# Optimization experiments

Measured on AMD Instinct MI355X. Metric: run time of the kernel, lower is better.

The kernel has to match this reference:

```python
import jax, jax.numpy as jnp
import numpy as np

ALPHA = 0.2  # leaky_relu negative slope
NEG = -1e12


def setup_inputs() -> dict:
    key = jax.random.key(0)
    k1, k2, k3, k4 = jax.random.split(key, 4)
    N, FIN, FOUT = 8192, 128, 64
    inp = jax.random.normal(k1, (N, FIN), dtype=jnp.float32)
    adj = jax.random.randint(k2, (N, N), 0, 2, dtype=jnp.int32)
    W = jax.random.normal(k3, (FIN, FOUT), dtype=jnp.float32) * 0.1
    a = jax.random.normal(k4, (2 * FOUT, 1), dtype=jnp.float32) * 0.1
    return {"inp": inp, "adj": adj, "W": W, "a": a}


def reference(inp, adj, W, a):
    # h: [N, F]
    h = inp @ W
    F = h.shape[1]
    # additive decomposition of a^T [h_i ; h_j] = (h @ a1)_i + (h @ a2)_j
    a1 = a[:F, 0]
    a2 = a[F:, 0]
    s1 = h @ a1  # [N]
    s2 = h @ a2  # [N]
    e = jax.nn.leaky_relu(s1[:, None] + s2[None, :], negative_slope=ALPHA)  # [N, N]
    att = jnp.where(adj > 0, e, jnp.float32(NEG))
    att = jax.nn.softmax(att, axis=1)
    # dropout is identity in eval mode (training=False)
    h_prime = att @ h  # [N, F]
    return jax.nn.elu(h_prime)  # concat=True
```

## Files before the change

kernel.cpp:

```cpp
#include <hip/hip_runtime.h>

typedef __attribute__((ext_vector_type(8))) short short8;
typedef __attribute__((ext_vector_type(4))) float f32x4;
typedef __attribute__((ext_vector_type(4))) int   i32x4;
typedef unsigned long long u64;

#define NN 8192
#define FIN 128
#define FOUT 64
#define LRELU_ALPHA 0.2f

__device__ __forceinline__ unsigned short f2bf(float x) {
    unsigned u = __float_as_uint(x);
    unsigned r = (u + 0x7FFFu + ((u >> 16) & 1u)) >> 16;
    return (unsigned short)r;
}

__device__ __forceinline__ unsigned vcol_of(unsigned i) {
    return (i & ~63u) | ((i & 3u) << 4) | ((i & 63u) >> 2);
}

__global__ __launch_bounds__(256) void gat_prep(
    const float* __restrict__ inp, const float* __restrict__ W,
    const float* __restrict__ a,
    unsigned short* __restrict__ htp, float* __restrict__ s1, float* __restrict__ s2,
    float* __restrict__ e1v, float* __restrict__ e2v)
{
    __shared__ float Wl[FIN * FOUT];
    __shared__ float il[4 * FIN];
    const int tid = threadIdx.x;
    const int i0 = blockIdx.x * 4;

    #pragma unroll
    for (int k = 0; k < (FIN * FOUT) / 256; ++k)
        Wl[tid + 256 * k] = W[tid + 256 * k];
    #pragma unroll
    for (int k = 0; k < (4 * FIN) / 256; ++k)
        il[tid + 256 * k] = inp[(size_t)i0 * FIN + tid + 256 * k];
    __syncthreads();

    const int r = tid >> 6;
    const int f = tid & 63;
    float acc = 0.f;
    #pragma unroll 8
    for (int k = 0; k < FIN; ++k)
        acc = fmaf(il[r * FIN + k], Wl[k * FOUT + f], acc);

    float v1 = acc * a[f];
    float v2 = acc * a[FOUT + f];
    #pragma unroll
    for (int off = 32; off; off >>= 1) {
        v1 += __shfl_xor(v1, off, 64);
        v2 += __shfl_xor(v2, off, 64);
    }
    const int i = i0 + r;
    const unsigned vc = vcol_of((unsigned)i);
    if (f == 0) {
        s1[i] = v1;
        s2[i] = v2;
        e1v[vc] = __expf(v2);
        e2v[vc] = __expf(LRELU_ALPHA * v2);
    }
    const unsigned Tt = vc >> 6, ic = vc & 63u;
    const unsigned ss = ic >> 5, kk = (ic >> 3) & 3u, ee = ic & 7u;
    const unsigned fb = (unsigned)f >> 4, ll = (unsigned)f & 15u;
    htp[((Tt * 8u + ss * 4u + fb) << 9) + ((kk * 16u + ll) << 3) + ee] = f2bf(acc);
}

__global__ __launch_bounds__(1024) void gat_s2max(const float* __restrict__ s2,
                                                  float* __restrict__ s2m)
{
    __shared__ float red[16];
    float m = -1e30f;
    for (int idx = threadIdx.x; idx < NN; idx += 1024) m = fmaxf(m, s2[idx]);
    #pragma unroll
    for (int off = 32; off; off >>= 1) m = fmaxf(m, __shfl_xor(m, off, 64));
    if ((threadIdx.x & 63) == 0) red[threadIdx.x >> 6] = m;
    __syncthreads();
    if (threadIdx.x == 0) {
        float mm = red[0];
        #pragma unroll
        for (int k = 1; k < 16; ++k) mm = fmaxf(mm, red[k]);
        s2m[0] = mm;
    }
}

#define ADJ_ISSUE(P, tt) do {                                                 \
    const unsigned oa_ = vadj0 + (unsigned)(tt) * 256u;                       \
    asm volatile("global_load_dwordx4 %0, %1, %2"                             \
                 : "=v"(P##0) : "v"(oa_), "s"(adjb));                         \
    asm volatile("global_load_dwordx4 %0, %1, %2"                             \
                 : "=v"(P##1) : "v"(oa_ + 131072u), "s"(adjb));               \
    asm volatile("global_load_dwordx4 %0, %1, %2"                             \
                 : "=v"(P##2) : "v"(oa_ + 262144u), "s"(adjb));               \
    asm volatile("global_load_dwordx4 %0, %1, %2"                             \
                 : "=v"(P##3) : "v"(oa_ + 393216u), "s"(adjb));               \
} while (0)

#define HTP_ISSUE(P, tt) do {                                                 \
    const unsigned oh_  = vhtp0 + (unsigned)(tt) * 8192u;                     \
    const unsigned oh2_ = oh_ + 4096u;                                        \
    asm volatile("global_load_dwordx4 %0, %1, %2 offset:0"                    \
                 : "=v"(P##_h0) : "v"(oh_), "s"(htpb));                       \
    asm volatile("global_load_dwordx4 %0, %1, %2 offset:1024"                 \
                 : "=v"(P##_h1) : "v"(oh_), "s"(htpb));                       \
    asm volatile("global_load_dwordx4 %0, %1, %2 offset:2048"                 \
                 : "=v"(P##_h2) : "v"(oh_), "s"(htpb));                       \
    asm volatile("global_load_dwordx4 %0, %1, %2 offset:3072"                 \
                 : "=v"(P##_h3) : "v"(oh_), "s"(htpb));                       \
    asm volatile("global_load_dwordx4 %0, %1, %2 offset:0"                    \
                 : "=v"(P##_h4) : "v"(oh2_), "s"(htpb));                      \
    asm volatile("global_load_dwordx4 %0, %1, %2 offset:1024"                 \
                 : "=v"(P##_h5) : "v"(oh2_), "s"(htpb));                      \
    asm volatile("global_load_dwordx4 %0, %1, %2 offset:2048"                 \
                 : "=v"(P##_h6) : "v"(oh2_), "s"(htpb));                      \
    asm volatile("global_load_dwordx4 %0, %1, %2 offset:3072"                 \
                 : "=v"(P##_h7) : "v"(oh2_), "s"(htpb));                      \
} while (0)

#define BALLOT1(V, rr, MBL, MBH) do {                                         \
    const u64 b0_ = __ballot(V[0] > 0);                                       \
    const u64 b1_ = __ballot(V[1] > 0);                                       \
    const u64 b2_ = __ballot(V[2] > 0);                                       \
    const u64 b3_ = __ballot(V[3] > 0);                                       \
    const u64 sA_ = (kg & 2) ? b1_ : b0_;                                     \
    const u64 sB_ = (kg & 2) ? b3_ : b2_;                                     \
    const unsigned m0_ = (unsigned)(sA_ >> sh) & 0xffu;                       \
    const unsigned m1_ = (unsigned)(sB_ >> sh) & 0xffu;                       \
    MBL = (myr == (rr)) ? m0_ : MBL;                                          \
    MBH = (myr == (rr)) ? m1_ : MBH;                                          \
} while (0)

#define BALLOT4(P, MBL, MBH) do {                                             \
    BALLOT1(P##0, 0, MBL, MBH);                                               \
    BALLOT1(P##1, 1, MBL, MBH);                                               \
    BALLOT1(P##2, 2, MBL, MBH);                                               \
    BALLOT1(P##3, 3, MBL, MBH);                                               \
} while (0)

#define COMPUTE(B0_, B1_, B2_, B3_, MB, uu) do {                              \
    const int eo_ = (uu) * 32 + 8 * kg;                                       \
    const f32x4 E1a_ = *(const f32x4*)&e1l[eo_];                              \
    const f32x4 E1b_ = *(const f32x4*)&e1l[eo_ + 4];                          \
    const f32x4 E2a_ = *(const f32x4*)&e2l[eo_];                              \
    const f32x4 E2b_ = *(const f32x4*)&e2l[eo_ + 4];                          \
    float p_[8];                                                              \
    _Pragma("unroll")                                                         \
    for (int e = 0; e < 8; ++e) {                                             \
        const float e1_ = (e < 4) ? E1a_[e] : E1b_[e - 4];                    \
        const float e2_ = (e < 4) ? E2a_[e] : E2b_[e - 4];                    \
        const float pv_ = fmaxf(c1 * e1_, c2 * e2_);                          \
        p_[e] = (((MB) >> e) & 1u) ? pv_ : 0.f;                               \
        lsum += p_[e];                                                        \
    }                                                                         \
    union { short8 s8; unsigned u4[4]; } afu_;                                \
    _Pragma("unroll")                                                         \
    for (int q = 0; q < 4; ++q) {                                             \
        unsigned rr_;                                                         \
        asm("v_cvt_pk_bf16_f32 %0, %1, %2"                                    \
            : "=v"(rr_) : "v"(p_[2 * q]), "v"(p_[2 * q + 1]));                \
        afu_.u4[q] = rr_;                                                     \
    }                                                                         \
    acc0 = __builtin_amdgcn_mfma_f32_16x16x32_bf16(afu_.s8, B0_, acc0, 0,0,0);\
    acc1 = __builtin_amdgcn_mfma_f32_16x16x32_bf16(afu_.s8, B1_, acc1, 0,0,0);\
    acc2 = __builtin_amdgcn_mfma_f32_16x16x32_bf16(afu_.s8, B2_, acc2, 0,0,0);\
    acc3 = __builtin_amdgcn_mfma_f32_16x16x32_bf16(afu_.s8, B3_, acc3, 0,0,0);\
} while (0)

#define ITER(P, tt, W) do {                                                   \
    asm volatile("s_waitcnt vmcnt(" #W ")" ::: "memory");                     \
    __builtin_amdgcn_sched_barrier(0);                                        \
    unsigned mbl_ = 0, mbh_ = 0;                                              \
    BALLOT4(P, mbl_, mbh_);                                                   \
    if ((tt) + 2 < nt) ADJ_ISSUE(P, (tt) + 2);                                \
    COMPUTE(P##_h0, P##_h1, P##_h2, P##_h3, mbl_, 2 * (tt));                  \
    COMPUTE(P##_h4, P##_h5, P##_h6, P##_h7, mbh_, 2 * (tt) + 1);              \
    if ((tt) + 2 < nt) HTP_ISSUE(P, (tt) + 2);                                \
} while (0)

__global__ __launch_bounds__(256, 2) void gat_attn(
    const int* __restrict__ adj, const unsigned short* __restrict__ htp,
    const float* __restrict__ s1, const float* __restrict__ e1v,
    const float* __restrict__ e2v, const float* __restrict__ s2m,
    float* __restrict__ pacc, float* __restrict__ pl, int jlen)
{
    __shared__ float e1l[2048];
    __shared__ float e2l[2048];

    const int w    = threadIdx.x >> 6;
    const int lane = threadIdx.x & 63;
    const int lo   = lane & 15;
    const int kg   = lane >> 4;
    const int i0   = blockIdx.x * 64;
    const int i    = i0 + w * 16 + lo;
    const int jstart = blockIdx.y * jlen;
    const int nt     = jlen >> 6;

    for (int x = threadIdx.x; x < (jlen >> 2); x += 256) {
        ((f32x4*)e1l)[x] = *(const f32x4*)(e1v + jstart + 4 * x);
        ((f32x4*)e2l)[x] = *(const f32x4*)(e2v + jstart + 4 * x);
    }
    __syncthreads();

    const float s1v = s1[i];
    const float mm  = s1v + s2m[0];
    const float Mi  = fmaxf(mm, LRELU_ALPHA * mm);
    const float c1  = __expf(s1v - Mi);
    const float c2  = __expf(LRELU_ALPHA * s1v - Mi);

    const int      myr = lo >> 2;
    const unsigned sh  = ((lo & 3) << 4) | ((kg & 1) << 3);

    const int* adjb = adj + (size_t)i0 * NN;
    const unsigned short* htpb = htp;
    const unsigned vadj0 = (unsigned)((((w * 16 + kg) * NN) + (lane & 15) * 4 + jstart) * 4);
    const unsigned vhtp0 = (unsigned)(((unsigned)(jstart >> 6) * 8192u) + lane * 16);

    f32x4 acc0 = {0.f,0.f,0.f,0.f}, acc1 = {0.f,0.f,0.f,0.f};
    f32x4 acc2 = {0.f,0.f,0.f,0.f}, acc3 = {0.f,0.f,0.f,0.f};
    float lsum = 0.f;

    i32x4 X0, X1, X2, X3, Y0, Y1, Y2, Y3;
    short8 X_h0, X_h1, X_h2, X_h3, X_h4, X_h5, X_h6, X_h7;
    short8 Y_h0, Y_h1, Y_h2, Y_h3, Y_h4, Y_h5, Y_h6, Y_h7;

    __builtin_amdgcn_sched_barrier(0);
    ADJ_ISSUE(X, 0); HTP_ISSUE(X, 0);
    ADJ_ISSUE(Y, 1); HTP_ISSUE(Y, 1);

    for (int k2 = 0; k2 < nt / 2 - 1; ++k2) {
        const int t0 = 2 * k2;
        ITER(X, t0, 12);
        ITER(Y, t0 + 1, 12);
    }
    ITER(X, nt - 2, 12);
    ITER(Y, nt - 1, 0);

    lsum += __shfl_xor(lsum, 16, 64);
    lsum += __shfl_xor(lsum, 32, 64);
    if (kg == 0)
        pl[(size_t)blockIdx.y * NN + i] = lsum;

    float* pa = pacc + ((size_t)blockIdx.y * NN + i0 + w * 16) * FOUT;
    #pragma unroll
    for (int reg = 0; reg < 4; ++reg) {
        const int orow = kg * 4 + reg;
        pa[(size_t)orow * FOUT + 0 * 16 + lo] = acc0[reg];
        pa[(size_t)orow * FOUT + 1 * 16 + lo] = acc1[reg];
        pa[(size_t)orow * FOUT + 2 * 16 + lo] = acc2[reg];
        pa[(size_t)orow * FOUT + 3 * 16 + lo] = acc3[reg];
    }
}

__global__ __launch_bounds__(256) void gat_reduce(
    const float* __restrict__ pacc, const float* __restrict__ pl,
    float* __restrict__ out, int JS)
{
    const int q = blockIdx.x * 256 + threadIdx.x;
    const int i = q >> 4;
    float l = 0.f;
    f32x4 v = {0.f, 0.f, 0.f, 0.f};
    for (int js = 0; js < JS; ++js) {
        l += pl[(size_t)js * NN + i];
        const f32x4 pv = *(const f32x4*)(pacc + (size_t)js * NN * FOUT + 4 * q);
        v[0] += pv[0]; v[1] += pv[1]; v[2] += pv[2]; v[3] += pv[3];
    }
    const float rl = 1.f / l;
    f32x4 o;
    #pragma unroll
    for (int e = 0; e < 4; ++e) {
        const float r = v[e] * rl;
        o[e] = r > 0.f ? r : expm1f(r);
    }
    *(f32x4*)(out + 4 * q) = o;
}

extern "C" void kernel_launch(void* const* d_in, const int* in_sizes, int n_in,
                              void* d_out, int out_size, void* d_ws, size_t ws_size,
                              hipStream_t stream)
{
    const float* inp = (const float*)d_in[0];
    const int*   adj = (const int*)d_in[1];
    const float* W   = (const float*)d_in[2];
    const float* a   = (const float*)d_in[3];
    float* out = (float*)d_out;

    char* ws = (char*)d_ws;
    unsigned short* htp = (unsigned short*)ws; ws += (size_t)FOUT * NN * 2;
    float* s1  = (float*)ws; ws += (size_t)NN * 4;
    float* s2  = (float*)ws; ws += (size_t)NN * 4;
    float* e1v = (float*)ws; ws += (size_t)NN * 4;
    float* e2v = (float*)ws; ws += (size_t)NN * 4;
    float* s2m = (float*)ws; ws += 256;
    const size_t fixed = (size_t)(ws - (char*)d_ws);

    int JS = 8;
    while (JS > 4 && fixed + (size_t)JS * NN * 4ull * (FOUT + 1) > ws_size) JS >>= 1;
    const int jlen = NN / JS;

    float* pl   = (float*)ws; ws += (size_t)JS * NN * 4;
    float* pacc = (float*)ws;

    gat_prep  <<<NN / 4, 256, 0, stream>>>(inp, W, a, htp, s1, s2, e1v, e2v);
    gat_s2max <<<1, 1024, 0, stream>>>(s2, s2m);
    gat_attn  <<<dim3(NN / 64, JS), 256, 0, stream>>>(adj, htp, s1, e1v, e2v, s2m, pacc, pl, jlen);
    gat_reduce<<<(NN * FOUT) / 1024, 256, 0, stream>>>(pacc, pl, out, JS);
}
```

Baseline: 87.30 us.

## Stage h tiles through LDS with direct global-to-LDS loads shared across waves

The attention kernel no longer has every wave load the full bf16 h tile into its own registers. Each wave now issues two direct global-to-LDS loads into a four-slot shared buffer, and all four waves read their MFMA B operands from LDS. This cuts redundant global traffic and register pressure, which may allow two blocks per CU. The cost is a workgroup barrier every iteration and LDS read traffic. The workspace-size fallback is removed and JS is fixed at 8, which could overflow a workspace that is too small.

```diff
diff --git a/kernel.cpp b/kernel.cpp
--- a/kernel.cpp
+++ b/kernel.cpp
@@ -14,6 +14,12 @@
     unsigned u = __float_as_uint(x);
     unsigned r = (u + 0x7FFFu + ((u >> 16) & 1u)) >> 16;
     return (unsigned short)r;
+}
+
+__device__ __forceinline__ void gl_lds16(const void* g, void* l) {
+    __builtin_amdgcn_global_load_lds(
+        (const __attribute__((address_space(1))) void*)g,
+        (__attribute__((address_space(3))) void*)l, 16, 0, 0);
 }
 
 __device__ __forceinline__ unsigned vcol_of(unsigned i) {
@@ -97,25 +103,12 @@
                  : "=v"(P##3) : "v"(oa_ + 393216u), "s"(adjb));               \
 } while (0)
 
-#define HTP_ISSUE(P, tt) do {                                                 \
-    const unsigned oh_  = vhtp0 + (unsigned)(tt) * 8192u;                     \
-    const unsigned oh2_ = oh_ + 4096u;                                        \
-    asm volatile("global_load_dwordx4 %0, %1, %2 offset:0"                    \
-                 : "=v"(P##_h0) : "v"(oh_), "s"(htpb));                       \
-    asm volatile("global_load_dwordx4 %0, %1, %2 offset:1024"                 \
-                 : "=v"(P##_h1) : "v"(oh_), "s"(htpb));                       \
-    asm volatile("global_load_dwordx4 %0, %1, %2 offset:2048"                 \
-                 : "=v"(P##_h2) : "v"(oh_), "s"(htpb));                       \
-    asm volatile("global_load_dwordx4 %0, %1, %2 offset:3072"                 \
-                 : "=v"(P##_h3) : "v"(oh_), "s"(htpb));                       \
-    asm volatile("global_load_dwordx4 %0, %1, %2 offset:0"                    \
-                 : "=v"(P##_h4) : "v"(oh2_), "s"(htpb));                      \
-    asm volatile("global_load_dwordx4 %0, %1, %2 offset:1024"                 \
-                 : "=v"(P##_h5) : "v"(oh2_), "s"(htpb));                      \
-    asm volatile("global_load_dwordx4 %0, %1, %2 offset:2048"                 \
-                 : "=v"(P##_h6) : "v"(oh2_), "s"(htpb));                      \
-    asm volatile("global_load_dwordx4 %0, %1, %2 offset:3072"                 \
-                 : "=v"(P##_h7) : "v"(oh2_), "s"(htpb));                      \
+#define ISSUE(P, tt) do {                                                     \
+    ADJ_ISSUE(P, tt);                                                         \
+    const unsigned short* g0_ = htpt + (size_t)(tt) * 4096 + (w * 2) * 512    \
+                                + lane * 8;                                   \
+    gl_lds16(g0_,       &hbuf[(tt) & 3][(w * 2) * 512]);                      \
+    gl_lds16(g0_ + 512, &hbuf[(tt) & 3][(w * 2 + 1) * 512]);                  \
 } while (0)
 
 #define BALLOT1(V, rr, MBL, MBH) do {                                         \
@@ -138,12 +131,16 @@
     BALLOT1(P##3, 3, MBL, MBH);                                               \
 } while (0)
 
-#define COMPUTE(B0_, B1_, B2_, B3_, MB, uu) do {                              \
+#define COMPUTE(HB, SB, MB, uu) do {                                          \
     const int eo_ = (uu) * 32 + 8 * kg;                                       \
     const f32x4 E1a_ = *(const f32x4*)&e1l[eo_];                              \
     const f32x4 E1b_ = *(const f32x4*)&e1l[eo_ + 4];                          \
     const f32x4 E2a_ = *(const f32x4*)&e2l[eo_];                              \
     const f32x4 E2b_ = *(const f32x4*)&e2l[eo_ + 4];                          \
+    const short8 B0_ = *(const short8*)((HB) + ((SB) * 4 + 0) * 512 + lane * 8); \
+    const short8 B1_ = *(const short8*)((HB) + ((SB) * 4 + 1) * 512 + lane * 8); \
+    const short8 B2_ = *(const short8*)((HB) + ((SB) * 4 + 2) * 512 + lane * 8); \
+    const short8 B3_ = *(const short8*)((HB) + ((SB) * 4 + 3) * 512 + lane * 8); \
     float p_[8];                                                              \
     _Pragma("unroll")                                                         \
     for (int e = 0; e < 8; ++e) {                                             \
@@ -170,12 +167,14 @@
 #define ITER(P, tt, W) do {                                                   \
     asm volatile("s_waitcnt vmcnt(" #W ")" ::: "memory");                     \
     __builtin_amdgcn_sched_barrier(0);                                        \
+    asm volatile("s_barrier" ::: "memory");                                   \
+    __builtin_amdgcn_sched_barrier(0);                                        \
     unsigned mbl_ = 0, mbh_ = 0;                                              \
     BALLOT4(P, mbl_, mbh_);                                                   \
-    if ((tt) + 2 < nt) ADJ_ISSUE(P, (tt) + 2);                                \
-    COMPUTE(P##_h0, P##_h1, P##_h2, P##_h3, mbl_, 2 * (tt));                  \
-    COMPUTE(P##_h4, P##_h5, P##_h6, P##_h7, mbh_, 2 * (tt) + 1);              \
-    if ((tt) + 2 < nt) HTP_ISSUE(P, (tt) + 2);                                \
+    const unsigned short* hb_ = &hbuf[(tt) & 3][0];                           \
+    COMPUTE(hb_, 0, mbl_, 2 * (tt));                                          \
+    COMPUTE(hb_, 1, mbh_, 2 * (tt) + 1);                                      \
+    if ((tt) + 2 < nt) ISSUE(P, (tt) + 2);                                    \
 } while (0)
 
 __global__ __launch_bounds__(256, 2) void gat_attn(
@@ -184,8 +183,9 @@
     const float* __restrict__ e2v, const float* __restrict__ s2m,
     float* __restrict__ pacc, float* __restrict__ pl, int jlen)
 {
-    __shared__ float e1l[2048];
-    __shared__ float e2l[2048];
+    __shared__ float e1l[1024];
+    __shared__ float e2l[1024];
+    __shared__ unsigned short hbuf[4][4096];
 
     const int w    = threadIdx.x >> 6;
     const int lane = threadIdx.x & 63;
@@ -212,28 +212,25 @@
     const unsigned sh  = ((lo & 3) << 4) | ((kg & 1) << 3);
 
     const int* adjb = adj + (size_t)i0 * NN;
-    const unsigned short* htpb = htp;
+    const unsigned short* htpt = htp + (size_t)(jstart >> 6) * 4096;
     const unsigned vadj0 = (unsigned)((((w * 16 + kg) * NN) + (lane & 15) * 4 + jstart) * 4);
-    const unsigned vhtp0 = (unsigned)(((unsigned)(jstart >> 6) * 8192u) + lane * 16);
 
     f32x4 acc0 = {0.f,0.f,0.f,0.f}, acc1 = {0.f,0.f,0.f,0.f};
     f32x4 acc2 = {0.f,0.f,0.f,0.f}, acc3 = {0.f,0.f,0.f,0.f};
     float lsum = 0.f;
 
     i32x4 X0, X1, X2, X3, Y0, Y1, Y2, Y3;
-    short8 X_h0, X_h1, X_h2, X_h3, X_h4, X_h5, X_h6, X_h7;
-    short8 Y_h0, Y_h1, Y_h2, Y_h3, Y_h4, Y_h5, Y_h6, Y_h7;
 
     __builtin_amdgcn_sched_barrier(0);
-    ADJ_ISSUE(X, 0); HTP_ISSUE(X, 0);
-    ADJ_ISSUE(Y, 1); HTP_ISSUE(Y, 1);
+    ISSUE(X, 0);
+    ISSUE(Y, 1);
 
     for (int k2 = 0; k2 < nt / 2 - 1; ++k2) {
         const int t0 = 2 * k2;
-        ITER(X, t0, 12);
-        ITER(Y, t0 + 1, 12);
-    }
-    ITER(X, nt - 2, 12);
+        ITER(X, t0, 6);
+        ITER(Y, t0 + 1, 6);
+    }
+    ITER(X, nt - 2, 6);
     ITER(Y, nt - 1, 0);
 
     lsum += __shfl_xor(lsum, 16, 64);
@@ -292,10 +289,8 @@
     float* e1v = (float*)ws; ws += (size_t)NN * 4;
     float* e2v = (float*)ws; ws += (size_t)NN * 4;
     float* s2m = (float*)ws; ws += 256;
-    const size_t fixed = (size_t)(ws - (char*)d_ws);
-
-    int JS = 8;
-    while (JS > 4 && fixed + (size_t)JS * NN * 4ull * (FOUT + 1) > ws_size) JS >>= 1;
+
+    const int JS = 8;
     const int jlen = NN / JS;
 
     float* pl   = (float*)ws; ws += (size_t)JS * NN * 4;
```

Result: slower. 91.49 us (+4.8%).
